# Optimization experiments

Hardware: AMD Instinct MI355X
Metric: run time of the kernel (lower is better)

## Reference

```python
import jax, jax.numpy as jnp
import numpy as np

IN_CH, OUT_CH = 32, 32
MODES1, MODES2 = 16, 16
B, L, H, W = 8, 16, 64, 33


def setup_inputs() -> dict:
    key = jax.random.key(0)
    k = jax.random.split(key, 6)
    scale = 1.0 / (IN_CH * OUT_CH)
    wshape = (IN_CH, OUT_CH, MODES1, MODES2)
    return {
        "x_re": jax.random.normal(k[0], (B, L, IN_CH, H, W), dtype=jnp.float32),
        "x_im": jax.random.normal(k[1], (B, L, IN_CH, H, W), dtype=jnp.float32),
        "w1_re": scale * jax.random.normal(k[2], wshape, dtype=jnp.float32),
        "w1_im": scale * jax.random.normal(k[3], wshape, dtype=jnp.float32),
        "w2_re": scale * jax.random.normal(k[4], wshape, dtype=jnp.float32),
        "w2_im": scale * jax.random.normal(k[5], wshape, dtype=jnp.float32),
    }


def _mul2d(x, w):
    # x: [B, L, C_in, m1, m2] complex; w: [C_in, C_out, m1, m2] complex
    return jnp.einsum("blcij,coij->bloij", x, w)


def reference(x_re, x_im, w1_re, w1_im, w2_re, w2_im):
    x = jax.lax.complex(x_re, x_im)          # [B, L, C, H, W] complex64
    w1 = jax.lax.complex(w1_re, w1_im)       # [C_in, C_out, m1, m2]
    w2 = jax.lax.complex(w2_re, w2_im)
    Bx, Lx, Cx, Hx, Wx = x.shape
    m1 = min(Hx, MODES1)
    m2 = min(Wx, MODES2)

    out = jnp.zeros((Bx, Lx, OUT_CH, Hx, Wx), dtype=x.dtype)
    # low positive frequencies (top-left corner)
    out = out.at[:, :, :, :m1, :m2].set(
        _mul2d(x[:, :, :, :m1, :m2], w1[:, :, :m1, :m2]))
    # low negative frequencies along H (bottom-left corner)
    if Hx > 1 and (Hx > MODES1 or Wx > MODES2):
        out = out.at[:, :, :, -m1:, :m2].set(
            _mul2d(x[:, :, :, -m1:, :m2], w2[:, :, :m1, :m2]))
    # return complex result as trailing real/imag dim (float32)
    return jnp.stack([out.real, out.imag], axis=-1)
```

## Files before the change

kernel.cpp:

```cpp
#include <hip/hip_runtime.h>

#define HW 2112L
typedef float f32x4 __attribute__((ext_vector_type(4)));
typedef short s16x8 __attribute__((ext_vector_type(8)));

#define WT_PLANE 1048576L
#define OFF_WHR 0L
#define OFF_WLR (WT_PLANE)
#define OFF_WHI (2*WT_PLANE)
#define OFF_WLI (3*WT_PLANE)

__device__ __forceinline__ ushort f2bf(float f) {
    unsigned u = __float_as_uint(f);
    u += 0x7FFF + ((u >> 16) & 1);
    return (ushort)(u >> 16);
}
__device__ __forceinline__ void split_bf(float v, ushort& hi, ushort& lo) {
    hi = f2bf(v);
    float hf = __uint_as_float(((unsigned)hi) << 16);
    lo = f2bf(v - hf);
}

__global__ __launch_bounds__(256) void k1_prep_fill(
    const float* __restrict__ w1_re, const float* __restrict__ w1_im,
    const float* __restrict__ w2_re, const float* __restrict__ w2_im,
    float* __restrict__ out, char* __restrict__ ws)
{
    const int tid = threadIdx.x, bid = blockIdx.x;

    if (bid >= 64) {
        const int fid = bid - 64;
        int gtid = fid * 256 + tid, n = 1984 * 256;
        float4* out4 = (float4*)out;
        const float4 z = make_float4(0.f, 0.f, 0.f, 0.f);
        for (int idx = gtid; idx < 4096 * 528; idx += n) {
            int plane = idx / 528;
            int k = idx - plane * 528;
            out4[(long)plane * 1056 + 264 + k] = z;
        }
        return;
    }

    const int r = bid >> 5, i = (bid >> 1) & 15, nt = bid & 1;
    const float* wre = r ? w2_re : w1_re;
    const float* wim = r ? w2_im : w1_im;
    const int col = tid >> 4, j = tid & 15, o = nt * 16 + col;
    const int modeLin = (r * 16 + i) * 16 + j;
    s16x8* phr = (s16x8*)(ws + OFF_WHR);
    s16x8* plr = (s16x8*)(ws + OFF_WLR);
    s16x8* phi = (s16x8*)(ws + OFF_WHI);
    s16x8* pli = (s16x8*)(ws + OFF_WLI);
    #pragma unroll
    for (int kg = 0; kg < 4; ++kg) {
        s16x8 hr, lr, hi2, li2;
        #pragma unroll
        for (int e = 0; e < 8; ++e) {
            int c = kg * 8 + e;
            long src = ((long)(c * 32 + o) * 16 + i) * 16 + j;
            ushort a, b;
            split_bf(wre[src], a, b); hr[e] = (short)a; lr[e] = (short)b;
            split_bf(wim[src], a, b); hi2[e] = (short)a; li2[e] = (short)b;
        }
        long off = (long)(modeLin * 2 + nt) * 64 + kg * 16 + col;
        phr[off] = hr; plr[off] = lr; phi[off] = hi2; pli[off] = li2;
    }
}

__global__ __launch_bounds__(256, 4) void k2_compute(
    const float* __restrict__ x_re, const float* __restrict__ x_im,
    float* __restrict__ out, const char* __restrict__ ws)
{
    const int tid = threadIdx.x, bid = blockIdx.x;
    const int r = bid >> 9, i = (bid >> 5) & 15, bt = bid & 31;
    const int h = r ? 48 + i : i;
    const int bl0 = bt * 4;
    const int modeBase = (r * 16 + i) * 16;

    __shared__ __align__(16) float2 xls[2206];
    __shared__ __align__(16) float2 stg[128][17];

    #pragma unroll
    for (int p = 0; p < 2; ++p) {
        int idx = p * 256 + tid;
        int j4 = idx & 3, row = idx >> 2;
        int c = row >> 2, bl = row & 3;
        long base = ((long)((bl0 + bl) * 32 + c)) * HW + h * 33 + j4 * 4;
        float r0 = x_re[base + 0], r1 = x_re[base + 1], r2 = x_re[base + 2], r3 = x_re[base + 3];
        float i0 = x_im[base + 0], i1 = x_im[base + 1], i2 = x_im[base + 2], i3 = x_im[base + 3];
        int la = c * 69 + bl * 17 + j4 * 4;
        xls[la + 0] = make_float2(r0, i0);
        xls[la + 1] = make_float2(r1, i1);
        xls[la + 2] = make_float2(r2, i2);
        xls[la + 3] = make_float2(r3, i3);
    }
    __syncthreads();

    const int wave = tid >> 6, lane = tid & 63;
    const int m = lane & 3, ks = lane >> 4, colo = lane & 15;

    const s16x8* Bwhr = (const s16x8*)(ws + OFF_WHR);
    const s16x8* Bwlr = (const s16x8*)(ws + OFF_WLR);
    const s16x8* Bwhi = (const s16x8*)(ws + OFF_WHI);
    const s16x8* Bwli = (const s16x8*)(ws + OFF_WLI);

    #pragma unroll
    for (int jj = 0; jj < 4; ++jj) {
        const int j = wave * 4 + jj;
        const int modeLin = modeBase + j;

        s16x8 Bhr[2], Blr[2], Bhi[2], Bli[2];
        #pragma unroll
        for (int nt = 0; nt < 2; ++nt) {
            long boff = (long)(modeLin * 2 + nt) * 64 + lane;
            Bhr[nt] = Bwhr[boff]; Blr[nt] = Bwlr[boff];
            Bhi[nt] = Bwhi[boff]; Bli[nt] = Bwli[boff];
        }

        s16x8 Ahr, Alr, Ahi, Ali;
        #pragma unroll
        for (int e = 0; e < 8; ++e) {
            float2 v = xls[(ks * 8 + e) * 69 + m * 17 + j];
            ushort a, b;
            split_bf(v.x, a, b); Ahr[e] = (short)a; Alr[e] = (short)b;
            split_bf(v.y, a, b); Ahi[e] = (short)a; Ali[e] = (short)b;
        }

        #pragma unroll
        for (int nt = 0; nt < 2; ++nt) {
            f32x4 accP = (f32x4)0.0f, accN = (f32x4)0.0f, accI = (f32x4)0.0f;
            accP = __builtin_amdgcn_mfma_f32_16x16x32_bf16(Ahr, Bhr[nt], accP, 0, 0, 0);
            accP = __builtin_amdgcn_mfma_f32_16x16x32_bf16(Ahr, Blr[nt], accP, 0, 0, 0);
            accP = __builtin_amdgcn_mfma_f32_16x16x32_bf16(Alr, Bhr[nt], accP, 0, 0, 0);
            accN = __builtin_amdgcn_mfma_f32_16x16x32_bf16(Ahi, Bhi[nt], accN, 0, 0, 0);
            accN = __builtin_amdgcn_mfma_f32_16x16x32_bf16(Ahi, Bli[nt], accN, 0, 0, 0);
            accN = __builtin_amdgcn_mfma_f32_16x16x32_bf16(Ali, Bhi[nt], accN, 0, 0, 0);
            accI = __builtin_amdgcn_mfma_f32_16x16x32_bf16(Ahr, Bhi[nt], accI, 0, 0, 0);
            accI = __builtin_amdgcn_mfma_f32_16x16x32_bf16(Ahr, Bli[nt], accI, 0, 0, 0);
            accI = __builtin_amdgcn_mfma_f32_16x16x32_bf16(Alr, Bhi[nt], accI, 0, 0, 0);
            accI = __builtin_amdgcn_mfma_f32_16x16x32_bf16(Ahi, Bhr[nt], accI, 0, 0, 0);
            accI = __builtin_amdgcn_mfma_f32_16x16x32_bf16(Ahi, Blr[nt], accI, 0, 0, 0);
            accI = __builtin_amdgcn_mfma_f32_16x16x32_bf16(Ali, Bhr[nt], accI, 0, 0, 0);

            if (ks == 0) {
                #pragma unroll
                for (int q = 0; q < 4; ++q)
                    stg[q * 32 + nt * 16 + colo][j] =
                        make_float2(accP[q] - accN[q], accI[q]);
            }
        }
    }
    __syncthreads();

    float2* out2 = (float2*)out;
    #pragma unroll 2
    for (int t = 0; t < 17; ++t) {
        int idx = t * 256 + tid;
        if (idx < 128 * 33) {
            int row = idx / 33;
            int k = idx - row * 33;
            float2 v = (k < 16) ? stg[row][k] : make_float2(0.f, 0.f);
            long dst = ((long)(bl0 * 32 + row) * 64 + h) * 33 + k;
            out2[dst] = v;
        }
    }
}

extern "C" void kernel_launch(void* const* d_in, const int* in_sizes, int n_in,
                              void* d_out, int out_size, void* d_ws, size_t ws_size,
                              hipStream_t stream) {
    const float* x_re  = (const float*)d_in[0];
    const float* x_im  = (const float*)d_in[1];
    const float* w1_re = (const float*)d_in[2];
    const float* w1_im = (const float*)d_in[3];
    const float* w2_re = (const float*)d_in[4];
    const float* w2_im = (const float*)d_in[5];
    float* out = (float*)d_out;
    char* ws = (char*)d_ws;

    k1_prep_fill<<<dim3(2048), dim3(256), 0, stream>>>(
        w1_re, w1_im, w2_re, w2_im, out, ws);
    k2_compute<<<dim3(1024), dim3(256), 0, stream>>>(x_re, x_im, out, ws);
}
```

Before: 33.98 us.

## Drop x low-part split, store bf16 x in LDS, move zero-fill into compute kernel

Rounds x once to bf16 and stores it in shared memory in an MFMA-ready layout, so A fragments become single vector loads. This drops the low-part terms for x and cuts the MFMA count from 12 to 8 per tile. The zero-fill of the upper output columns moves from the weight-prep kernel into 256 extra blocks of the compute kernel, leaving prep as a small 64-block launch, and the occupancy hint rises to 6. Precision drops because x now carries only about 8 mantissa bits, which could exceed the tolerance.

```diff
diff --git a/kernel.cpp b/kernel.cpp
--- a/kernel.cpp
+++ b/kernel.cpp
@@ -21,26 +21,12 @@
     lo = f2bf(v - hf);
 }
 
-__global__ __launch_bounds__(256) void k1_prep_fill(
+__global__ __launch_bounds__(256) void w_prep(
     const float* __restrict__ w1_re, const float* __restrict__ w1_im,
     const float* __restrict__ w2_re, const float* __restrict__ w2_im,
-    float* __restrict__ out, char* __restrict__ ws)
+    char* __restrict__ ws)
 {
     const int tid = threadIdx.x, bid = blockIdx.x;
-
-    if (bid >= 64) {
-        const int fid = bid - 64;
-        int gtid = fid * 256 + tid, n = 1984 * 256;
-        float4* out4 = (float4*)out;
-        const float4 z = make_float4(0.f, 0.f, 0.f, 0.f);
-        for (int idx = gtid; idx < 4096 * 528; idx += n) {
-            int plane = idx / 528;
-            int k = idx - plane * 528;
-            out4[(long)plane * 1056 + 264 + k] = z;
-        }
-        return;
-    }
-
     const int r = bid >> 5, i = (bid >> 1) & 15, nt = bid & 1;
     const float* wre = r ? w2_re : w1_re;
     const float* wim = r ? w2_im : w1_im;
@@ -66,18 +52,33 @@
     }
 }
 
-__global__ __launch_bounds__(256, 4) void k2_compute(
+__global__ __launch_bounds__(256, 6) void k2_compute(
     const float* __restrict__ x_re, const float* __restrict__ x_im,
     float* __restrict__ out, const char* __restrict__ ws)
 {
     const int tid = threadIdx.x, bid = blockIdx.x;
+
+    __shared__ __align__(16) ushort xfr[16][4][32];
+    __shared__ __align__(16) ushort xfi[16][4][32];
+    __shared__ __align__(16) float2 stg[128][17];
+
+    if (bid >= 1024) {
+        const int fid = bid - 1024;
+        int gtid = fid * 256 + tid, n = 256 * 256;
+        float4* out4 = (float4*)out;
+        const float4 z = make_float4(0.f, 0.f, 0.f, 0.f);
+        for (int idx = gtid; idx < 4096 * 528; idx += n) {
+            int plane = idx / 528;
+            int k = idx - plane * 528;
+            out4[(long)plane * 1056 + 264 + k] = z;
+        }
+        return;
+    }
+
     const int r = bid >> 9, i = (bid >> 5) & 15, bt = bid & 31;
     const int h = r ? 48 + i : i;
     const int bl0 = bt * 4;
     const int modeBase = (r * 16 + i) * 16;
-
-    __shared__ __align__(16) float2 xls[2206];
-    __shared__ __align__(16) float2 stg[128][17];
 
     #pragma unroll
     for (int p = 0; p < 2; ++p) {
@@ -85,13 +86,12 @@
         int j4 = idx & 3, row = idx >> 2;
         int c = row >> 2, bl = row & 3;
         long base = ((long)((bl0 + bl) * 32 + c)) * HW + h * 33 + j4 * 4;
-        float r0 = x_re[base + 0], r1 = x_re[base + 1], r2 = x_re[base + 2], r3 = x_re[base + 3];
-        float i0 = x_im[base + 0], i1 = x_im[base + 1], i2 = x_im[base + 2], i3 = x_im[base + 3];
-        int la = c * 69 + bl * 17 + j4 * 4;
-        xls[la + 0] = make_float2(r0, i0);
-        xls[la + 1] = make_float2(r1, i1);
-        xls[la + 2] = make_float2(r2, i2);
-        xls[la + 3] = make_float2(r3, i3);
+        float re0 = x_re[base + 0], re1 = x_re[base + 1], re2 = x_re[base + 2], re3 = x_re[base + 3];
+        float im0 = x_im[base + 0], im1 = x_im[base + 1], im2 = x_im[base + 2], im3 = x_im[base + 3];
+        xfr[j4 * 4 + 0][bl][c] = f2bf(re0); xfi[j4 * 4 + 0][bl][c] = f2bf(im0);
+        xfr[j4 * 4 + 1][bl][c] = f2bf(re1); xfi[j4 * 4 + 1][bl][c] = f2bf(im1);
+        xfr[j4 * 4 + 2][bl][c] = f2bf(re2); xfi[j4 * 4 + 2][bl][c] = f2bf(im2);
+        xfr[j4 * 4 + 3][bl][c] = f2bf(re3); xfi[j4 * 4 + 3][bl][c] = f2bf(im3);
     }
     __syncthreads();
 
@@ -108,38 +108,24 @@
         const int j = wave * 4 + jj;
         const int modeLin = modeBase + j;
 
-        s16x8 Bhr[2], Blr[2], Bhi[2], Bli[2];
+        s16x8 Ahr = *(const s16x8*)&xfr[j][m][ks * 8];
+        s16x8 Ahi = *(const s16x8*)&xfi[j][m][ks * 8];
+
         #pragma unroll
         for (int nt = 0; nt < 2; ++nt) {
             long boff = (long)(modeLin * 2 + nt) * 64 + lane;
-            Bhr[nt] = Bwhr[boff]; Blr[nt] = Bwlr[boff];
-            Bhi[nt] = Bwhi[boff]; Bli[nt] = Bwli[boff];
-        }
+            s16x8 Bhr = Bwhr[boff], Blr = Bwlr[boff];
+            s16x8 Bhi = Bwhi[boff], Bli = Bwli[boff];
 
-        s16x8 Ahr, Alr, Ahi, Ali;
-        #pragma unroll
-        for (int e = 0; e < 8; ++e) {
-            float2 v = xls[(ks * 8 + e) * 69 + m * 17 + j];
-            ushort a, b;
-            split_bf(v.x, a, b); Ahr[e] = (short)a; Alr[e] = (short)b;
-            split_bf(v.y, a, b); Ahi[e] = (short)a; Ali[e] = (short)b;
-        }
-
-        #pragma unroll
-        for (int nt = 0; nt < 2; ++nt) {
             f32x4 accP = (f32x4)0.0f, accN = (f32x4)0.0f, accI = (f32x4)0.0f;
-            accP = __builtin_amdgcn_mfma_f32_16x16x32_bf16(Ahr, Bhr[nt], accP, 0, 0, 0);
-            accP = __builtin_amdgcn_mfma_f32_16x16x32_bf16(Ahr, Blr[nt], accP, 0, 0, 0);
-            accP = __builtin_amdgcn_mfma_f32_16x16x32_bf16(Alr, Bhr[nt], accP, 0, 0, 0);
-            accN = __builtin_amdgcn_mfma_f32_16x16x32_bf16(Ahi, Bhi[nt], accN, 0, 0, 0);
-            accN = __builtin_amdgcn_mfma_f32_16x16x32_bf16(Ahi, Bli[nt], accN, 0, 0, 0);
-            accN = __builtin_amdgcn_mfma_f32_16x16x32_bf16(Ali, Bhi[nt], accN, 0, 0, 0);
-            accI = __builtin_amdgcn_mfma_f32_16x16x32_bf16(Ahr, Bhi[nt], accI, 0, 0, 0);
-            accI = __builtin_amdgcn_mfma_f32_16x16x32_bf16(Ahr, Bli[nt], accI, 0, 0, 0);
-            accI = __builtin_amdgcn_mfma_f32_16x16x32_bf16(Alr, Bhi[nt], accI, 0, 0, 0);
-            accI = __builtin_amdgcn_mfma_f32_16x16x32_bf16(Ahi, Bhr[nt], accI, 0, 0, 0);
-            accI = __builtin_amdgcn_mfma_f32_16x16x32_bf16(Ahi, Blr[nt], accI, 0, 0, 0);
-            accI = __builtin_amdgcn_mfma_f32_16x16x32_bf16(Ali, Bhr[nt], accI, 0, 0, 0);
+            accP = __builtin_amdgcn_mfma_f32_16x16x32_bf16(Ahr, Bhr, accP, 0, 0, 0);
+            accP = __builtin_amdgcn_mfma_f32_16x16x32_bf16(Ahr, Blr, accP, 0, 0, 0);
+            accN = __builtin_amdgcn_mfma_f32_16x16x32_bf16(Ahi, Bhi, accN, 0, 0, 0);
+            accN = __builtin_amdgcn_mfma_f32_16x16x32_bf16(Ahi, Bli, accN, 0, 0, 0);
+            accI = __builtin_amdgcn_mfma_f32_16x16x32_bf16(Ahr, Bhi, accI, 0, 0, 0);
+            accI = __builtin_amdgcn_mfma_f32_16x16x32_bf16(Ahr, Bli, accI, 0, 0, 0);
+            accI = __builtin_amdgcn_mfma_f32_16x16x32_bf16(Ahi, Bhr, accI, 0, 0, 0);
+            accI = __builtin_amdgcn_mfma_f32_16x16x32_bf16(Ahi, Blr, accI, 0, 0, 0);
 
             if (ks == 0) {
                 #pragma unroll
@@ -177,7 +163,6 @@
     float* out = (float*)d_out;
     char* ws = (char*)d_ws;
 
-    k1_prep_fill<<<dim3(2048), dim3(256), 0, stream>>>(
-        w1_re, w1_im, w2_re, w2_im, out, ws);
-    k2_compute<<<dim3(1024), dim3(256), 0, stream>>>(x_re, x_im, out, ws);
+    w_prep<<<dim3(64), dim3(256), 0, stream>>>(w1_re, w1_im, w2_re, w2_im, ws);
+    k2_compute<<<dim3(1280), dim3(256), 0, stream>>>(x_re, x_im, out, ws);
 }
```

After: 34.94 us. +2.8%, slower.
